# Kernel optimization log

Measured on AMD Instinct MI355X. Metric: run time of the kernel, lower is better.

Reference implementation:

```python
import jax, jax.numpy as jnp
import numpy as np

NEIGH_W = 0.25  # self.neigh_w
act = jax.nn.leaky_relu  # negative_slope=0.01, matches nn.LeakyReLU default


def _lin(x, w, b):
    # torch Linear with weight stored as [in, out]
    return x @ w + b


def setup_inputs() -> dict:
    key = jax.random.key(0)
    I, C, L = 1024, 32, 64  # images, curves/image, points/curve (uniform segments)
    N = I * C * L
    ks = jax.random.split(key, 32)

    def p(k, shape, scale=0.1):
        return jax.random.normal(k, shape, dtype=jnp.float32) * scale

    curve_tensor = jax.random.normal(ks[0], (N, 8), dtype=jnp.float32)
    # segment-boundary labels: col1 = curve start (every L rows), col0 = image start (every L*C rows)
    lab = np.zeros((N, 2), np.int64)
    lab[::L, 1] = 1
    lab[::L * C, 0] = 1
    curve_label = jnp.asarray(lab)
    cors_batch = jax.random.normal(ks[1], (I, C, C, 5), dtype=jnp.float32)

    inp = dict(curve_tensor=curve_tensor, curve_label=curve_label, cors_batch=cors_batch)
    dims = [("crv_mlp", 8, 8), ("crv_lv1", 24, 32), ("crv_lv2", 32, 24),
            ("inter1", 24, 24), ("inter2", 24, 24),
            ("grp1", 72, 24), ("grp2", 24, 24), ("grp3", 24, 24),
            ("img1", 24, 18), ("img2", 18, 12), ("img3", 12, 6)]
    for i, (name, din, dout) in enumerate(dims):
        inp[name + "_w"] = p(ks[2 + 2 * i], (din, dout))
        inp[name + "_b"] = p(ks[3 + 2 * i], (dout,))
    # cor_mlp is initialized to all ones (cor_init_rand=0 in the original)
    inp["cor_w"] = jnp.ones((5, 24), jnp.float32)
    inp["cor_b"] = jnp.ones((24,), jnp.float32)
    return inp


def reference(curve_tensor, curve_label, cors_batch,
              crv_mlp_w, crv_mlp_b, crv_lv1_w, crv_lv1_b, crv_lv2_w, crv_lv2_b,
              inter1_w, inter1_b, inter2_w, inter2_b, cor_w, cor_b,
              grp1_w, grp1_b, grp2_w, grp2_b, grp3_w, grp3_b,
              img1_w, img1_b, img2_w, img2_b, img3_w, img3_b):
    I, C = cors_batch.shape[0], cors_batch.shape[1]
    L = curve_tensor.shape[0] // (I * C)

    # ---- curve level: ring-graph roll aggregation within each curve segment ----
    x = curve_tensor.reshape(I * C, L, 8)

    def agg(t):
        neigh = _lin(jnp.roll(t, 1, axis=1), crv_mlp_w, crv_mlp_b) \
              + _lin(jnp.roll(t, -1, axis=1), crv_mlp_w, crv_mlp_b)
        return NEIGH_W * neigh + (1.0 - 2.0 * NEIGH_W) * t

    x1 = agg(x)
    x2 = agg(x1)
    embed = jnp.concatenate([x, x1, x2], axis=-1)            # [I*C, L, 24]
    feat = act(_lin(act(_lin(embed, crv_lv1_w, crv_lv1_b)), crv_lv2_w, crv_lv2_b))
    group = feat.mean(axis=1)                                 # [I*C, 24] per-curve feature
    group = act(_lin(act(_lin(group, inter1_w, inter1_b)), inter2_w, inter2_b))

    # ---- image level: pairwise cor-weighted aggregation over curves per image ----
    g = group.reshape(I, C, 24)
    cor = act(_lin(cors_batch, cor_w, cor_b))                 # [I, C, C, 24]

    def cagg(t):
        # after[i,j,d] = sum_k before[i,k,d] * cor[i,j,k,d]
        return jnp.einsum('ikd,ijkd->ijd', t, cor)

    g1 = cagg(g)
    g2 = cagg(g1)
    emb = jnp.concatenate([g, g1, g2], axis=-1)               # [I, C, 72]
    h = act(_lin(act(_lin(act(_lin(emb, grp1_w, grp1_b)), grp2_w, grp2_b)), grp3_w, grp3_b))
    img = h.mean(axis=1)                                      # [I, 24]

    out = _lin(act(_lin(act(_lin(img, img1_w, img1_b)), img2_w, img2_b)), img3_w, img3_b)
    return jax.nn.sigmoid(out)                                # [I, brands]
```

## Files before the change

### kernel.cpp

```cpp
#include <hip/hip_runtime.h>
#include <hip/hip_bf16.h>
#include <math.h>

#define LEAKY(x) fmaxf((x), 0.01f * (x))

typedef float v2f __attribute__((ext_vector_type(2)));
typedef __bf16 bf8 __attribute__((ext_vector_type(8)));
typedef float f4 __attribute__((ext_vector_type(4)));

constexpr int IMGS = 1024;
constexpr int CRV  = 32;
constexpr int LPT  = 64;

__device__ __forceinline__ void ldseg(float* dst, const float* __restrict__ src,
                                      int n, int tid, int nt) {
  for (int i = tid; i < n; i += nt) dst[i] = src[i];
}

__device__ __forceinline__ f4 leaky4(f4 x) {
  return __builtin_elementwise_max(x, x * 0.01f);
}

__device__ __forceinline__ float ring_sum(float v) {
  int s = __builtin_bit_cast(int, v);
  int a = __builtin_amdgcn_update_dpp(0, s, 0x134, 0xF, 0xF, false);
  int b = __builtin_amdgcn_update_dpp(0, s, 0x13C, 0xF, 0xF, false);
  return __builtin_bit_cast(float, a) + __builtin_bit_cast(float, b);
}

__device__ __forceinline__ float row_sum16(float v) {
  int s;
  s = __builtin_amdgcn_update_dpp(0, __builtin_bit_cast(int, v), 0x121, 0xF, 0xF, false);
  v += __builtin_bit_cast(float, s);
  s = __builtin_amdgcn_update_dpp(0, __builtin_bit_cast(int, v), 0x122, 0xF, 0xF, false);
  v += __builtin_bit_cast(float, s);
  s = __builtin_amdgcn_update_dpp(0, __builtin_bit_cast(int, v), 0x124, 0xF, 0xF, false);
  v += __builtin_bit_cast(float, s);
  s = __builtin_amdgcn_update_dpp(0, __builtin_bit_cast(int, v), 0x128, 0xF, 0xF, false);
  v += __builtin_bit_cast(float, s);
  return v;
}

__device__ __forceinline__ unsigned bfpair(float x, float y) {
  __hip_bfloat162 h = __float22bfloat162_rn(make_float2(x, y));
  unsigned r;
  __builtin_memcpy(&r, &h, 4);
  return r;
}

__device__ __forceinline__ unsigned bfr(float x) {
  unsigned u = __builtin_bit_cast(unsigned, x);
  return u + 0x7fffu + ((u >> 16) & 1u);
}
__device__ __forceinline__ unsigned bfpair_fast(float x, float y) {
  return __builtin_amdgcn_perm(bfr(y), bfr(x), 0x07060302u);
}

#define WOFF(pp, cc) (((pp) << 4) + ((((cc) + ((pp) >> 1)) & 3) << 2))

__device__ float w1eff_val(const float* mw, const float* mb,
                           const float* w1, const float* b1, int n, int k) {
  if (k < 8) {
    return w1[k * 32 + n] + 0.5f * w1[(8 + k) * 32 + n] + 0.25f * w1[(16 + k) * 32 + n];
  } else if (k < 16) {
    int a = k - 8;
    float s = 0.f;
    for (int i = 0; i < 8; i++)
      s += mw[a * 8 + i] * (w1[(8 + i) * 32 + n] + w1[(16 + i) * 32 + n]);
    return 0.25f * s;
  } else if (k < 24) {
    int a = k - 16;
    float s = 0.f;
    for (int i = 0; i < 8; i++) {
      float m2 = 0.f;
      for (int c = 0; c < 8; c++) m2 += mw[a * 8 + c] * mw[c * 8 + i];
      s += m2 * w1[(16 + i) * 32 + n];
    }
    return 0.0625f * s;
  } else if (k == 24) {
    float s = b1[n];
    for (int i = 0; i < 8; i++) {
      s += mb[i] * (0.5f * w1[(8 + i) * 32 + n] + 0.75f * w1[(16 + i) * 32 + n]);
      float wb = 0.f;
      for (int c = 0; c < 8; c++) wb += mb[c] * mw[c * 8 + i];
      s += 0.25f * wb * w1[(16 + i) * 32 + n];
    }
    return s;
  }
  return 0.f;
}

__global__ __launch_bounds__(256) void prep_kernel(
    const float* __restrict__ mw, const float* __restrict__ mb,
    const float* __restrict__ w1, const float* __restrict__ b1,
    const float* __restrict__ w2, const float* __restrict__ b2,
    const float* __restrict__ i1w, const float* __restrict__ i2w,
    unsigned* __restrict__ fragA1, unsigned* __restrict__ fragA2,
    float* __restrict__ fragC,
    float* __restrict__ i1wT, float* __restrict__ i2wT)
{
  const int tid = threadIdx.x;
  for (int idx = tid; idx < 512; idx += 256) {
    int tile = idx >> 8;
    int lane = (idx >> 2) & 63;
    int word = idx & 3;
    int n  = tile * 16 + (lane & 15);
    int k0 = (lane >> 4) * 8 + word * 2;
    fragA1[idx] = bfpair(w1eff_val(mw, mb, w1, b1, n, k0),
                         w1eff_val(mw, mb, w1, b1, n, k0 + 1));
    float u0 = (n < 24) ? w2[k0 * 24 + n] : 0.f;
    float u1 = (n < 24) ? w2[(k0 + 1) * 24 + n] : 0.f;
    fragA2[idx] = bfpair(u0, u1);
  }
  for (int idx = tid; idx < 512; idx += 256) {
    int tile = idx >> 8;
    int lane = (idx >> 2) & 63;
    int r = idx & 3;
    int n = tile * 16 + ((lane >> 4) & 3) * 4 + r;
    fragC[idx] = (n < 24) ? b2[n] : 0.f;
  }
  for (int idx = tid; idx < 576; idx += 256) {
    int jj = idx / 24, ii = idx - jj * 24;
    i1wT[idx] = i1w[ii * 24 + jj];
    i2wT[idx] = i2w[ii * 24 + jj];
  }
}

__global__ __launch_bounds__(256) void curve_kernel(
    const float* __restrict__ ct,
    const unsigned* __restrict__ fragA1, const unsigned* __restrict__ fragA2,
    const float* __restrict__ fragC,
    const float* __restrict__ i1wT, const float* __restrict__ i1b,
    const float* __restrict__ i2wT, const float* __restrict__ i2b,
    float* __restrict__ gout)
{
  __shared__ __align__(16) unsigned sX[4][1024];
  __shared__ __align__(16) float    srow[4][32];

  const int tid  = threadIdx.x;
  const int wave = tid >> 6;
  const int lane = tid & 63;
  const int curve = blockIdx.x * 4 + wave;

  uint4 awv[2], a2v[2];
  float4 cbv[2];
  #pragma unroll
  for (int mt = 0; mt < 2; mt++) {
    awv[mt] = *(const uint4*)(fragA1 + mt * 256 + lane * 4);
    a2v[mt] = *(const uint4*)(fragA2 + mt * 256 + lane * 4);
    cbv[mt] = *(const float4*)(fragC + mt * 256 + lane * 4);
  }

  const float* p = ct + ((size_t)curve * LPT + lane) * 8;
  float4 t0 = *(const float4*)p;
  float4 t1 = *(const float4*)(p + 4);
  float x[8];
  x[0] = t0.x; x[1] = t0.y; x[2] = t0.z; x[3] = t0.w;
  x[4] = t1.x; x[5] = t1.y; x[6] = t1.z; x[7] = t1.w;
  float s1[8], t2[8];
  #pragma unroll
  for (int i = 0; i < 8; i++) s1[i] = ring_sum(x[i]);
  #pragma unroll
  for (int i = 0; i < 8; i++) t2[i] = ring_sum(s1[i]);

  unsigned* Xw = &sX[wave][0];
  {
    uint4 wv;
    wv.x = bfpair_fast(x[0], x[1]);  wv.y = bfpair_fast(x[2], x[3]);
    wv.z = bfpair_fast(x[4], x[5]);  wv.w = bfpair_fast(x[6], x[7]);
    *(uint4*)&Xw[WOFF(lane, 0)] = wv;
    wv.x = bfpair_fast(s1[0], s1[1]); wv.y = bfpair_fast(s1[2], s1[3]);
    wv.z = bfpair_fast(s1[4], s1[5]); wv.w = bfpair_fast(s1[6], s1[7]);
    *(uint4*)&Xw[WOFF(lane, 1)] = wv;
    wv.x = bfpair_fast(t2[0], t2[1]); wv.y = bfpair_fast(t2[2], t2[3]);
    wv.z = bfpair_fast(t2[4], t2[5]); wv.w = bfpair_fast(t2[6], t2[7]);
    *(uint4*)&Xw[WOFF(lane, 2)] = wv;
    wv.x = 0x00003f80u; wv.y = 0u; wv.z = 0u; wv.w = 0u;
    *(uint4*)&Xw[WOFF(lane, 3)] = wv;
  }
  __builtin_amdgcn_wave_barrier();

  const int q   = lane >> 4;
  const int c16 = lane & 15;

  f4 d[2][4];
  {
    bf8 bx[4];
    #pragma unroll
    for (int nt = 0; nt < 4; nt++)
      bx[nt] = __builtin_bit_cast(bf8, *(const uint4*)&Xw[WOFF(c16 + nt * 16, q)]);
    const f4 z = (f4){0.f, 0.f, 0.f, 0.f};
    #pragma unroll
    for (int mt = 0; mt < 2; mt++) {
      bf8 aw = __builtin_bit_cast(bf8, awv[mt]);
      #pragma unroll
      for (int nt = 0; nt < 4; nt++)
        d[mt][nt] = __builtin_amdgcn_mfma_f32_16x16x32_bf16(aw, bx[nt], z, 0, 0, 0);
    }
  }
  #pragma unroll
  for (int mt = 0; mt < 2; mt++) {
    #pragma unroll
    for (int nt = 0; nt < 4; nt++) {
      f4 v = leaky4(d[mt][nt]);
      const int prow = nt * 16 + c16;
      const int word = WOFF(prow, mt * 2 + (q >> 1)) + (q & 1) * 2;
      uint2 pk; pk.x = bfpair_fast(v.x, v.y); pk.y = bfpair_fast(v.z, v.w);
      *(uint2*)&Xw[word] = pk;
    }
  }
  __builtin_amdgcn_wave_barrier();

  f4 d2[2][4];
  {
    bf8 bh[4];
    #pragma unroll
    for (int nt = 0; nt < 4; nt++)
      bh[nt] = __builtin_bit_cast(bf8, *(const uint4*)&Xw[WOFF(c16 + nt * 16, q)]);
    #pragma unroll
    for (int mt = 0; mt < 2; mt++) {
      bf8 a2 = __builtin_bit_cast(bf8, a2v[mt]);
      f4 cb_ = __builtin_bit_cast(f4, cbv[mt]);
      #pragma unroll
      for (int nt = 0; nt < 4; nt++)
        d2[mt][nt] = __builtin_amdgcn_mfma_f32_16x16x32_bf16(a2, bh[nt], cb_, 0, 0, 0);
    }
  }

  float m8[2][4];
  #pragma unroll
  for (int mt = 0; mt < 2; mt++) {
    f4 t = leaky4(d2[mt][0]) + leaky4(d2[mt][1]);
    t = t + leaky4(d2[mt][2]);
    t = t + leaky4(d2[mt][3]);
    #pragma unroll
    for (int r = 0; r < 4; r++)
      m8[mt][r] = row_sum16(t[r]) * (1.0f / 64.0f);
  }
  if (c16 == 0) {
    f4 v0 = (f4){m8[0][0], m8[0][1], m8[0][2], m8[0][3]};
    *(f4*)&srow[wave][q * 4] = v0;
    if (q < 2) {
      f4 v1 = (f4){m8[1][0], m8[1][1], m8[1][2], m8[1][3]};
      *(f4*)&srow[wave][16 + q * 4] = v1;
    }
  }
  __builtin_amdgcn_wave_barrier();

  float sv[24];
  #pragma unroll
  for (int i = 0; i < 24; i++) sv[i] = srow[wave][i];

  const int jd = (lane < 24) ? lane : 0;
  float a = i1b[jd];
  #pragma unroll
  for (int t = 0; t < 6; t++) {
    float4 wv = *(const float4*)&i1wT[jd * 24 + t * 4];
    a += sv[t * 4 + 0] * wv.x + sv[t * 4 + 1] * wv.y
       + sv[t * 4 + 2] * wv.z + sv[t * 4 + 3] * wv.w;
  }
  a = LEAKY(a);
  if (lane < 24) srow[wave][lane] = a;
  __builtin_amdgcn_wave_barrier();

  float av[24];
  #pragma unroll
  for (int i = 0; i < 24; i++) av[i] = srow[wave][i];

  float o = i2b[jd];
  #pragma unroll
  for (int t = 0; t < 6; t++) {
    float4 wv = *(const float4*)&i2wT[jd * 24 + t * 4];
    o += av[t * 4 + 0] * wv.x + av[t * 4 + 1] * wv.y
       + av[t * 4 + 2] * wv.z + av[t * 4 + 3] * wv.w;
  }
  o = LEAKY(o);

  if (lane < 24) gout[(size_t)curve * 24 + lane] = o;
}

__global__ __launch_bounds__(768) void image_kernel(
    const float* __restrict__ cors, const float* __restrict__ gin,
    const float* __restrict__ cw,  const float* __restrict__ cb,
    const float* __restrict__ g1w, const float* __restrict__ g1b,
    const float* __restrict__ g2w, const float* __restrict__ g2b,
    const float* __restrict__ g3w, const float* __restrict__ g3b,
    const float* __restrict__ m1w, const float* __restrict__ m1b,
    const float* __restrict__ m2w, const float* __restrict__ m2b,
    const float* __restrict__ m3w, const float* __restrict__ m3b,
    float* __restrict__ out)
{
  __shared__ __align__(16) float sCorsP[CRV * CRV * 8];
  __shared__ __align__(16) float sG0[CRV * 24], sG1[CRV * 24], sG2[CRV * 24];
  __shared__ __align__(16) float sHa[CRV * 24], sHb[CRV * 24];
  __shared__ float sW1[1728], sW2[576], sW3[576];
  __shared__ float sT[96];

  const int tid = threadIdx.x;
  const int img = blockIdx.x;
  const int j = tid / 24;
  const int d = tid - j * 24;

  {
    const float* cbase = cors + (size_t)img * (CRV * CRV * 5);
    for (int idx = tid; idx < CRV * CRV * 5; idx += 768) {
      int jj = idx / 160;
      int r  = idx - jj * 160;
      int k  = r / 5;
      int c  = r - k * 5;
      sCorsP[(jj * CRV + k) * 8 + c] = cbase[idx];
    }
  }
  sG0[tid] = gin[(size_t)img * (CRV * 24) + tid];
  ldseg(sW1, g1w, 1728, tid, 768);
  ldseg(sW2, g2w, 576, tid, 768);
  ldseg(sW3, g3w, 576, tid, 768);
  float wc0 = cw[0 * 24 + d], wc1 = cw[1 * 24 + d], wc2 = cw[2 * 24 + d];
  float wc3 = cw[3 * 24 + d], wc4 = cw[4 * 24 + d];
  float cbd = cb[d];
  float g1bd = g1b[d], g2bd = g2b[d], g3bd = g3b[d];
  __syncthreads();

  float corv[CRV];
  #pragma unroll
  for (int k = 0; k < CRV; k++) {
    const float* cr = &sCorsP[(j * CRV + k) * 8];
    float4 qq = *(const float4*)cr;
    float q4 = cr[4];
    float v = cbd + qq.x * wc0 + qq.y * wc1 + qq.z * wc2 + qq.w * wc3 + q4 * wc4;
    corv[k] = LEAKY(v);
  }
  {
    float t1 = 0.0f;
    #pragma unroll
    for (int k = 0; k < CRV; k++) t1 += sG0[k * 24 + d] * corv[k];
    sG1[j * 24 + d] = t1;
  }
  __syncthreads();
  {
    float t2 = 0.0f;
    #pragma unroll
    for (int k = 0; k < CRV; k++) t2 += sG1[k * 24 + d] * corv[k];
    sG2[j * 24 + d] = t2;
  }
  __syncthreads();
  {
    float v = g1bd;
    #pragma unroll
    for (int i = 0; i < 24; i++) v += sG0[j * 24 + i] * sW1[i * 24 + d];
    #pragma unroll
    for (int i = 0; i < 24; i++) v += sG1[j * 24 + i] * sW1[(24 + i) * 24 + d];
    #pragma unroll
    for (int i = 0; i < 24; i++) v += sG2[j * 24 + i] * sW1[(48 + i) * 24 + d];
    sHa[j * 24 + d] = LEAKY(v);
  }
  __syncthreads();
  {
    float v = g2bd;
    #pragma unroll
    for (int i = 0; i < 24; i++) v += sHa[j * 24 + i] * sW2[i * 24 + d];
    sHb[j * 24 + d] = LEAKY(v);
  }
  __syncthreads();
  {
    float v = g3bd;
    #pragma unroll
    for (int i = 0; i < 24; i++) v += sHb[j * 24 + i] * sW3[i * 24 + d];
    sHa[j * 24 + d] = LEAKY(v);
  }
  __syncthreads();
  if (tid < 24) {
    float s = 0.0f;
    #pragma unroll
    for (int k = 0; k < CRV; k++) s += sHa[k * 24 + tid];
    sT[tid] = s * (1.0f / CRV);
  }
  __syncthreads();
  if (tid < 18) {
    float v = m1b[tid];
    #pragma unroll
    for (int i = 0; i < 24; i++) v += sT[i] * m1w[i * 18 + tid];
    sT[32 + tid] = LEAKY(v);
  }
  __syncthreads();
  if (tid < 12) {
    float v = m2b[tid];
    #pragma unroll
    for (int i = 0; i < 18; i++) v += sT[32 + i] * m2w[i * 12 + tid];
    sT[56 + tid] = LEAKY(v);
  }
  __syncthreads();
  if (tid < 6) {
    float v = m3b[tid];
    #pragma unroll
    for (int i = 0; i < 12; i++) v += sT[56 + i] * m3w[i * 6 + tid];
    out[img * 6 + tid] = 1.0f / (1.0f + expf(-v));
  }
}

extern "C" void kernel_launch(void* const* d_in, const int* in_sizes, int n_in,
                              void* d_out, int out_size, void* d_ws, size_t ws_size,
                              hipStream_t stream) {
  const float* ct   = (const float*)d_in[0];
  const float* cors = (const float*)d_in[2];
  const float* mw  = (const float*)d_in[3];
  const float* mb  = (const float*)d_in[4];
  const float* w1  = (const float*)d_in[5];
  const float* b1  = (const float*)d_in[6];
  const float* w2  = (const float*)d_in[7];
  const float* b2  = (const float*)d_in[8];
  const float* i1w = (const float*)d_in[9];
  const float* i1b = (const float*)d_in[10];
  const float* i2w = (const float*)d_in[11];
  const float* i2b = (const float*)d_in[12];

  const float *cw, *cb, *g1w, *g1b, *g2w, *g2b, *g3w, *g3b;
  const float *m1w, *m1b, *m2w, *m2b, *m3w, *m3b;
  if (in_sizes[13] == 120) {
    cw  = (const float*)d_in[13]; cb  = (const float*)d_in[14];
    g1w = (const float*)d_in[15]; g1b = (const float*)d_in[16];
    g2w = (const float*)d_in[17]; g2b = (const float*)d_in[18];
    g3w = (const float*)d_in[19]; g3b = (const float*)d_in[20];
    m1w = (const float*)d_in[21]; m1b = (const float*)d_in[22];
    m2w = (const float*)d_in[23]; m2b = (const float*)d_in[24];
    m3w = (const float*)d_in[25]; m3b = (const float*)d_in[26];
  } else {
    g1w = (const float*)d_in[13]; g1b = (const float*)d_in[14];
    g2w = (const float*)d_in[15]; g2b = (const float*)d_in[16];
    g3w = (const float*)d_in[17]; g3b = (const float*)d_in[18];
    m1w = (const float*)d_in[19]; m1b = (const float*)d_in[20];
    m2w = (const float*)d_in[21]; m2b = (const float*)d_in[22];
    m3w = (const float*)d_in[23]; m3b = (const float*)d_in[24];
    cw  = (const float*)d_in[25]; cb  = (const float*)d_in[26];
  }

  float* wsf = (float*)d_ws;
  float* group = wsf;
  const size_t base = (size_t)IMGS * CRV * 24;
  unsigned* fragA1 = (unsigned*)(wsf + base);
  unsigned* fragA2 = fragA1 + 512;
  float*    fragC  = (float*)(fragA2 + 512);
  float*    i1wT   = fragC + 512;
  float*    i2wT   = i1wT + 576;
  float* out = (float*)d_out;

  prep_kernel<<<1, 256, 0, stream>>>(mw, mb, w1, b1, w2, b2, i1w, i2w,
                                     fragA1, fragA2, fragC, i1wT, i2wT);
  curve_kernel<<<(IMGS * CRV) / 4, 256, 0, stream>>>(
      ct, fragA1, fragA2, fragC, i1wT, i1b, i2wT, i2b, group);
  image_kernel<<<IMGS, 768, 0, stream>>>(
      cors, group, cw, cb, g1w, g1b, g2w, g2b, g3w, g3b,
      m1w, m1b, m2w, m2b, m3w, m3b, out);
}
```

Baseline: 227.7 us.

## Process two curves per wave in curve kernel to amortize fragment loads

Each wave now handles two curves instead of one, so the block covers eight curves and the grid is halved. The weight fragments loaded into registers are reused across both curves, and the inter MLP tail runs both curves at once using the two 32-lane halves of the wave, where before 40 lanes sat idle. The cost is double the LDS per block and more registers, which may lower occupancy, and there are fewer blocks to hide the latency of the global loads.

```diff
diff --git a/kernel.cpp b/kernel.cpp
--- a/kernel.cpp
+++ b/kernel.cpp
@@ -134,13 +134,13 @@
     const float* __restrict__ i2wT, const float* __restrict__ i2b,
     float* __restrict__ gout)
 {
-  __shared__ __align__(16) unsigned sX[4][1024];
-  __shared__ __align__(16) float    srow[4][32];
+  __shared__ __align__(16) unsigned sX[4][2][1024];
+  __shared__ __align__(16) float    srow[4][2][32];
 
   const int tid  = threadIdx.x;
   const int wave = tid >> 6;
   const int lane = tid & 63;
-  const int curve = blockIdx.x * 4 + wave;
+  const int curve0 = blockIdx.x * 8 + wave * 2;
 
   uint4 awv[2], a2v[2];
   float4 cbv[2];
@@ -151,40 +151,66 @@
     cbv[mt] = *(const float4*)(fragC + mt * 256 + lane * 4);
   }
 
-  const float* p = ct + ((size_t)curve * LPT + lane) * 8;
-  float4 t0 = *(const float4*)p;
-  float4 t1 = *(const float4*)(p + 4);
-  float x[8];
-  x[0] = t0.x; x[1] = t0.y; x[2] = t0.z; x[3] = t0.w;
-  x[4] = t1.x; x[5] = t1.y; x[6] = t1.z; x[7] = t1.w;
-  float s1[8], t2[8];
-  #pragma unroll
-  for (int i = 0; i < 8; i++) s1[i] = ring_sum(x[i]);
-  #pragma unroll
-  for (int i = 0; i < 8; i++) t2[i] = ring_sum(s1[i]);
-
-  unsigned* Xw = &sX[wave][0];
+  const float* pA = ct + ((size_t)curve0 * LPT + lane) * 8;
+  const float* pB = pA + LPT * 8;
+  float4 a0 = *(const float4*)pA;
+  float4 a1 = *(const float4*)(pA + 4);
+  float4 b0 = *(const float4*)pB;
+  float4 b1v = *(const float4*)(pB + 4);
+
+  float xA[8], xB[8];
+  xA[0] = a0.x; xA[1] = a0.y; xA[2] = a0.z; xA[3] = a0.w;
+  xA[4] = a1.x; xA[5] = a1.y; xA[6] = a1.z; xA[7] = a1.w;
+  xB[0] = b0.x; xB[1] = b0.y; xB[2] = b0.z; xB[3] = b0.w;
+  xB[4] = b1v.x; xB[5] = b1v.y; xB[6] = b1v.z; xB[7] = b1v.w;
+
+  float s1A[8], t2A[8], s1B[8], t2B[8];
+  #pragma unroll
+  for (int i = 0; i < 8; i++) s1A[i] = ring_sum(xA[i]);
+  #pragma unroll
+  for (int i = 0; i < 8; i++) s1B[i] = ring_sum(xB[i]);
+  #pragma unroll
+  for (int i = 0; i < 8; i++) t2A[i] = ring_sum(s1A[i]);
+  #pragma unroll
+  for (int i = 0; i < 8; i++) t2B[i] = ring_sum(s1B[i]);
+
+  unsigned* Xw0 = &sX[wave][0][0];
+  unsigned* Xw1 = &sX[wave][1][0];
   {
     uint4 wv;
-    wv.x = bfpair_fast(x[0], x[1]);  wv.y = bfpair_fast(x[2], x[3]);
-    wv.z = bfpair_fast(x[4], x[5]);  wv.w = bfpair_fast(x[6], x[7]);
-    *(uint4*)&Xw[WOFF(lane, 0)] = wv;
-    wv.x = bfpair_fast(s1[0], s1[1]); wv.y = bfpair_fast(s1[2], s1[3]);
-    wv.z = bfpair_fast(s1[4], s1[5]); wv.w = bfpair_fast(s1[6], s1[7]);
-    *(uint4*)&Xw[WOFF(lane, 1)] = wv;
-    wv.x = bfpair_fast(t2[0], t2[1]); wv.y = bfpair_fast(t2[2], t2[3]);
-    wv.z = bfpair_fast(t2[4], t2[5]); wv.w = bfpair_fast(t2[6], t2[7]);
-    *(uint4*)&Xw[WOFF(lane, 2)] = wv;
+    wv.x = bfpair_fast(xA[0], xA[1]);  wv.y = bfpair_fast(xA[2], xA[3]);
+    wv.z = bfpair_fast(xA[4], xA[5]);  wv.w = bfpair_fast(xA[6], xA[7]);
+    *(uint4*)&Xw0[WOFF(lane, 0)] = wv;
+    wv.x = bfpair_fast(s1A[0], s1A[1]); wv.y = bfpair_fast(s1A[2], s1A[3]);
+    wv.z = bfpair_fast(s1A[4], s1A[5]); wv.w = bfpair_fast(s1A[6], s1A[7]);
+    *(uint4*)&Xw0[WOFF(lane, 1)] = wv;
+    wv.x = bfpair_fast(t2A[0], t2A[1]); wv.y = bfpair_fast(t2A[2], t2A[3]);
+    wv.z = bfpair_fast(t2A[4], t2A[5]); wv.w = bfpair_fast(t2A[6], t2A[7]);
+    *(uint4*)&Xw0[WOFF(lane, 2)] = wv;
     wv.x = 0x00003f80u; wv.y = 0u; wv.z = 0u; wv.w = 0u;
-    *(uint4*)&Xw[WOFF(lane, 3)] = wv;
+    *(uint4*)&Xw0[WOFF(lane, 3)] = wv;
+
+    wv.x = bfpair_fast(xB[0], xB[1]);  wv.y = bfpair_fast(xB[2], xB[3]);
+    wv.z = bfpair_fast(xB[4], xB[5]);  wv.w = bfpair_fast(xB[6], xB[7]);
+    *(uint4*)&Xw1[WOFF(lane, 0)] = wv;
+    wv.x = bfpair_fast(s1B[0], s1B[1]); wv.y = bfpair_fast(s1B[2], s1B[3]);
+    wv.z = bfpair_fast(s1B[4], s1B[5]); wv.w = bfpair_fast(s1B[6], s1B[7]);
+    *(uint4*)&Xw1[WOFF(lane, 1)] = wv;
+    wv.x = bfpair_fast(t2B[0], t2B[1]); wv.y = bfpair_fast(t2B[2], t2B[3]);
+    wv.z = bfpair_fast(t2B[4], t2B[5]); wv.w = bfpair_fast(t2B[6], t2B[7]);
+    *(uint4*)&Xw1[WOFF(lane, 2)] = wv;
+    wv.x = 0x00003f80u; wv.y = 0u; wv.z = 0u; wv.w = 0u;
+    *(uint4*)&Xw1[WOFF(lane, 3)] = wv;
   }
   __builtin_amdgcn_wave_barrier();
 
   const int q   = lane >> 4;
   const int c16 = lane & 15;
 
-  f4 d[2][4];
-  {
+  #pragma unroll
+  for (int cv = 0; cv < 2; cv++) {
+    unsigned* Xw = cv ? Xw1 : Xw0;
+    f4 d[2][4];
     bf8 bx[4];
     #pragma unroll
     for (int nt = 0; nt < 4; nt++)
@@ -197,22 +223,24 @@
       for (int nt = 0; nt < 4; nt++)
         d[mt][nt] = __builtin_amdgcn_mfma_f32_16x16x32_bf16(aw, bx[nt], z, 0, 0, 0);
     }
-  }
-  #pragma unroll
-  for (int mt = 0; mt < 2; mt++) {
-    #pragma unroll
-    for (int nt = 0; nt < 4; nt++) {
-      f4 v = leaky4(d[mt][nt]);
-      const int prow = nt * 16 + c16;
-      const int word = WOFF(prow, mt * 2 + (q >> 1)) + (q & 1) * 2;
-      uint2 pk; pk.x = bfpair_fast(v.x, v.y); pk.y = bfpair_fast(v.z, v.w);
-      *(uint2*)&Xw[word] = pk;
+    #pragma unroll
+    for (int mt = 0; mt < 2; mt++) {
+      #pragma unroll
+      for (int nt = 0; nt < 4; nt++) {
+        f4 v = leaky4(d[mt][nt]);
+        const int prow = nt * 16 + c16;
+        const int word = WOFF(prow, mt * 2 + (q >> 1)) + (q & 1) * 2;
+        uint2 pk; pk.x = bfpair_fast(v.x, v.y); pk.y = bfpair_fast(v.z, v.w);
+        *(uint2*)&Xw[word] = pk;
+      }
     }
   }
   __builtin_amdgcn_wave_barrier();
 
-  f4 d2[2][4];
-  {
+  #pragma unroll
+  for (int cv = 0; cv < 2; cv++) {
+    unsigned* Xw = cv ? Xw1 : Xw0;
+    f4 d2[2][4];
     bf8 bh[4];
     #pragma unroll
     for (int nt = 0; nt < 4; nt++)
@@ -225,33 +253,36 @@
       for (int nt = 0; nt < 4; nt++)
         d2[mt][nt] = __builtin_amdgcn_mfma_f32_16x16x32_bf16(a2, bh[nt], cb_, 0, 0, 0);
     }
-  }
-
-  float m8[2][4];
-  #pragma unroll
-  for (int mt = 0; mt < 2; mt++) {
-    f4 t = leaky4(d2[mt][0]) + leaky4(d2[mt][1]);
-    t = t + leaky4(d2[mt][2]);
-    t = t + leaky4(d2[mt][3]);
-    #pragma unroll
-    for (int r = 0; r < 4; r++)
-      m8[mt][r] = row_sum16(t[r]) * (1.0f / 64.0f);
-  }
-  if (c16 == 0) {
-    f4 v0 = (f4){m8[0][0], m8[0][1], m8[0][2], m8[0][3]};
-    *(f4*)&srow[wave][q * 4] = v0;
-    if (q < 2) {
-      f4 v1 = (f4){m8[1][0], m8[1][1], m8[1][2], m8[1][3]};
-      *(f4*)&srow[wave][16 + q * 4] = v1;
+    float m8[2][4];
+    #pragma unroll
+    for (int mt = 0; mt < 2; mt++) {
+      f4 t = leaky4(d2[mt][0]) + leaky4(d2[mt][1]);
+      t = t + leaky4(d2[mt][2]);
+      t = t + leaky4(d2[mt][3]);
+      #pragma unroll
+      for (int r = 0; r < 4; r++)
+        m8[mt][r] = row_sum16(t[r]) * (1.0f / 64.0f);
+    }
+    if (c16 == 0) {
+      f4 v0 = (f4){m8[0][0], m8[0][1], m8[0][2], m8[0][3]};
+      *(f4*)&srow[wave][cv][q * 4] = v0;
+      if (q < 2) {
+        f4 v1 = (f4){m8[1][0], m8[1][1], m8[1][2], m8[1][3]};
+        *(f4*)&srow[wave][cv][16 + q * 4] = v1;
+      }
     }
   }
   __builtin_amdgcn_wave_barrier();
 
+  const int half = lane >> 5;
+  const int l32  = lane & 31;
+  const int jd   = (l32 < 24) ? l32 : 0;
+  float* srw = &srow[wave][half][0];
+
   float sv[24];
   #pragma unroll
-  for (int i = 0; i < 24; i++) sv[i] = srow[wave][i];
-
-  const int jd = (lane < 24) ? lane : 0;
+  for (int i = 0; i < 24; i++) sv[i] = srw[i];
+
   float a = i1b[jd];
   #pragma unroll
   for (int t = 0; t < 6; t++) {
@@ -260,12 +291,12 @@
        + sv[t * 4 + 2] * wv.z + sv[t * 4 + 3] * wv.w;
   }
   a = LEAKY(a);
-  if (lane < 24) srow[wave][lane] = a;
+  if (l32 < 24) srw[l32] = a;
   __builtin_amdgcn_wave_barrier();
 
   float av[24];
   #pragma unroll
-  for (int i = 0; i < 24; i++) av[i] = srow[wave][i];
+  for (int i = 0; i < 24; i++) av[i] = srw[i];
 
   float o = i2b[jd];
   #pragma unroll
@@ -276,7 +307,7 @@
   }
   o = LEAKY(o);
 
-  if (lane < 24) gout[(size_t)curve * 24 + lane] = o;
+  if (l32 < 24) gout[(size_t)(curve0 + half) * 24 + l32] = o;
 }
 
 __global__ __launch_bounds__(768) void image_kernel(
@@ -446,7 +477,7 @@
 
   prep_kernel<<<1, 256, 0, stream>>>(mw, mb, w1, b1, w2, b2, i1w, i2w,
                                      fragA1, fragA2, fragC, i1wT, i2wT);
-  curve_kernel<<<(IMGS * CRV) / 4, 256, 0, stream>>>(
+  curve_kernel<<<(IMGS * CRV) / 8, 256, 0, stream>>>(
       ct, fragA1, fragA2, fragC, i1wT, i1b, i2wT, i2b, group);
   image_kernel<<<IMGS, 768, 0, stream>>>(
       cors, group, cw, cb, g1w, g1b, g2w, g2b, g3w, g3b,
```

Result: faster. 220.0 us (-3.4%).
